# Performance work log

Hardware: AMD Instinct MI355X
Metric: run time of the kernel (lower is better)

The kernel has to match this reference:

```python
import jax, jax.numpy as jnp
import numpy as np

ALPHA = 0.2  # leaky relu slope
NEG_BIG = -9000000000000000.0


def setup_inputs() -> dict:
    key = jax.random.key(0)
    k1, k2, k3, k4 = jax.random.split(key, 4)
    B, N, Fin, Fout = 8, 2048, 256, 256
    h = jax.random.normal(k1, (B, N, Fin), dtype=jnp.float32)
    adj = jax.random.randint(k2, (B, N, N), 0, 2, dtype=jnp.int32)
    # xavier_uniform with gain=1.414
    gain = 1.414
    limW = gain * np.sqrt(6.0 / (Fin + Fout))
    W = jax.random.uniform(k3, (Fin, Fout), dtype=jnp.float32, minval=-limW, maxval=limW)
    lima = gain * np.sqrt(6.0 / (2 * Fout + 1))
    a = jax.random.uniform(k4, (2 * Fout, 1), dtype=jnp.float32, minval=-lima, maxval=lima)
    return {"h": h, "adj": adj, "W": W, "a": a}


def reference(h, adj, W, a):
    # Wh: [B, N, F]
    Wh = jnp.matmul(h, W)
    Fout = W.shape[1]
    a1 = a[:Fout, 0]   # scores for source node i (repeat_interleave side)
    a2 = a[Fout:, 0]   # scores for target node j (repeat side)
    # e[b,i,j] = leakyrelu(Wh[b,i]@a1 + Wh[b,j]@a2)  -- decomposed, no O(N^2 * 2F) tensor
    s1 = jnp.einsum('bnf,f->bn', Wh, a1)  # [B, N]
    s2 = jnp.einsum('bnf,f->bn', Wh, a2)  # [B, N]
    e = jax.nn.leaky_relu(s1[:, :, None] + s2[:, None, :], negative_slope=ALPHA)
    masked = jnp.where(adj > 0, e, jnp.full_like(e, NEG_BIG))
    attention = jax.nn.softmax(masked, axis=2)  # dropout=0 (eval mode)
    h_prime = jnp.matmul(attention, Wh)  # [B, N, F]
    return jax.nn.elu(h_prime)
```

## Files before the change

### kernel.cpp

```cpp
#include <hip/hip_runtime.h>

typedef __attribute__((ext_vector_type(8))) short bhalf8;
typedef __attribute__((ext_vector_type(4))) float floatx4;

#define ALPHA_LR 0.2f

__device__ __forceinline__ unsigned short f2bf(float f) {
  union { float f; unsigned int u; } v; v.f = f;
  unsigned int r = v.u + 0x7fffu + ((v.u >> 16) & 1u);
  return (unsigned short)(r >> 16);
}
__device__ __forceinline__ float bf2f(unsigned short u) {
  union { unsigned int u; float f; } v; v.u = ((unsigned int)u) << 16;
  return v.f;
}
__device__ __forceinline__ void gld16(const void* g, void* l) {
  __builtin_amdgcn_global_load_lds((const __attribute__((address_space(1))) unsigned int*)g,
                                   (__attribute__((address_space(3))) unsigned int*)l,
                                   16, 0, 0);
}

__global__ void k0w_split(const float* __restrict__ W,
                          unsigned short* __restrict__ WThi,
                          unsigned short* __restrict__ WTlo,
                          unsigned int* __restrict__ s2maxEnc) {
  __shared__ float s[16][17];
  const int tx = threadIdx.x, ty = threadIdx.y;
  if (blockIdx.x == 0 && blockIdx.y == 0 && ty == 0 && tx < 8) s2maxEnc[tx] = 0u;
  const int n0 = blockIdx.x * 16, k0 = blockIdx.y * 16;
  s[ty][tx] = W[(k0 + ty) * 256 + n0 + tx];
  __syncthreads();
  float v = s[tx][ty];
  const int k = k0 + tx, n = n0 + ty;
  unsigned short hi = f2bf(v);
  unsigned short lo = f2bf(v - bf2f(hi));
  const int idx = (k >> 5) * 8192 + n * 32 + (k & 31);
  WThi[idx] = hi;
  WTlo[idx] = lo;
}

__global__ __launch_bounds__(256) void k2_pack(const int* __restrict__ adj,
                                               unsigned long long* __restrict__ mask) {
  const int wave = threadIdx.x >> 6, lane = threadIdx.x & 63;
  const long wid = (long)blockIdx.x * 4 + wave;
  const long u0 = wid * 64;
  const int* base = adj + u0 * 64 + lane;
#pragma unroll
  for (int it = 0; it < 64; it += 4) {
    int v0 = base[(it + 0) * 64];
    int v1 = base[(it + 1) * 64];
    int v2 = base[(it + 2) * 64];
    int v3 = base[(it + 3) * 64];
    unsigned long long m0 = __ballot(v0 > 0);
    unsigned long long m1 = __ballot(v1 > 0);
    unsigned long long m2 = __ballot(v2 > 0);
    unsigned long long m3 = __ballot(v3 > 0);
    if (lane == 0) {
      mask[u0 + it + 0] = m0;
      mask[u0 + it + 1] = m1;
      mask[u0 + it + 2] = m2;
      mask[u0 + it + 3] = m3;
    }
  }
}

__global__ __launch_bounds__(512, 2) void k1_mfma(const float* __restrict__ h,
                                                  const unsigned short* __restrict__ Bhi_g,
                                                  const unsigned short* __restrict__ Blo_g,
                                                  const float* __restrict__ a_g,
                                                  unsigned short* __restrict__ WhPack,
                                                  float* __restrict__ s1,
                                                  float* __restrict__ s2,
                                                  unsigned int* __restrict__ s2maxEnc) {
  __shared__ unsigned short Ah[64 * 264], Al[64 * 264];
  __shared__ unsigned short Bh[2][8192], Bl[2][8192];
  __shared__ float s1red[64], s2red[64];
  const int t = threadIdx.x;
  const long r0 = (long)blockIdx.x * 64;
  const int wave = t >> 6, lane = t & 63;

  if (t < 64) { s1red[t] = 0.f; s2red[t] = 0.f; }

#pragma unroll
  for (int rep = 0; rep < 2; rep++) {
    const int off = wave * 1024 + rep * 512;
    gld16(Bhi_g + off + lane * 8, &Bh[0][off]);
    gld16(Blo_g + off + lane * 8, &Bl[0][off]);
  }

#pragma unroll
  for (int q = 0; q < 8; q++) {
    int idx = q * 512 + t;
    int row = idx >> 6, c4 = idx & 63;
    float4 x = *(const float4*)(h + (r0 + row) * 256 + c4 * 4);
    float xs[4] = {x.x, x.y, x.z, x.w};
    unsigned short hs[4], ls[4];
#pragma unroll
    for (int qq = 0; qq < 4; qq++) {
      hs[qq] = f2bf(xs[qq]);
      ls[qq] = f2bf(xs[qq] - bf2f(hs[qq]));
    }
    *(ushort4*)&Ah[row * 264 + c4 * 4] = (ushort4){hs[0], hs[1], hs[2], hs[3]};
    *(ushort4*)&Al[row * 264 + c4 * 4] = (ushort4){ls[0], ls[1], ls[2], ls[3]};
  }
  __syncthreads();

  const int wm = wave >> 2, wn = wave & 3;
  const int lhi = lane >> 4, llo = lane & 15;

  floatx4 acc[2][4];
#pragma unroll
  for (int mt = 0; mt < 2; mt++)
#pragma unroll
    for (int nt = 0; nt < 4; nt++) acc[mt][nt] = (floatx4){0.f, 0.f, 0.f, 0.f};

  for (int ks = 0; ks < 8; ks++) {
    const int cur = ks & 1, nxt = cur ^ 1, ksn = (ks + 1) & 7;
#pragma unroll
    for (int rep = 0; rep < 2; rep++) {
      const int off = wave * 1024 + rep * 512;
      gld16(Bhi_g + ksn * 8192 + off + lane * 8, &Bh[nxt][off]);
      gld16(Blo_g + ksn * 8192 + off + lane * 8, &Bl[nxt][off]);
    }

    const int k0 = ks * 32;
    bhalf8 ah[2], al[2], bh[4], bl[4];
#pragma unroll
    for (int mt = 0; mt < 2; mt++) {
      int ro = (wm * 32 + mt * 16 + llo) * 264 + k0 + lhi * 8;
      ah[mt] = *(const bhalf8*)&Ah[ro];
      al[mt] = *(const bhalf8*)&Al[ro];
    }
#pragma unroll
    for (int nt = 0; nt < 4; nt++) {
      int ro = (wn * 64 + nt * 16 + llo) * 32 + lhi * 8;
      bh[nt] = *(const bhalf8*)&Bh[cur][ro];
      bl[nt] = *(const bhalf8*)&Bl[cur][ro];
    }
#pragma unroll
    for (int mt = 0; mt < 2; mt++)
#pragma unroll
      for (int nt = 0; nt < 4; nt++) {
        acc[mt][nt] = __builtin_amdgcn_mfma_f32_16x16x32_bf16(ah[mt], bh[nt], acc[mt][nt], 0, 0, 0);
        acc[mt][nt] = __builtin_amdgcn_mfma_f32_16x16x32_bf16(ah[mt], bl[nt], acc[mt][nt], 0, 0, 0);
        acc[mt][nt] = __builtin_amdgcn_mfma_f32_16x16x32_bf16(al[mt], bh[nt], acc[mt][nt], 0, 0, 0);
      }
    __syncthreads();
  }

  float a1v[4], a2v[4];
#pragma unroll
  for (int nt = 0; nt < 4; nt++) {
    int f = wn * 64 + nt * 16 + llo;
    a1v[nt] = a_g[f];
    a2v[nt] = a_g[256 + f];
  }

  const int b = (int)(r0 >> 11);
  const int jt_base = (int)((r0 & 2047) >> 5);

#pragma unroll
  for (int mt = 0; mt < 2; mt++) {
    float p1[4], p2[4];
#pragma unroll
    for (int reg = 0; reg < 4; reg++) {
      p1[reg] = acc[mt][0][reg] * a1v[0] + acc[mt][1][reg] * a1v[1] +
                acc[mt][2][reg] * a1v[2] + acc[mt][3][reg] * a1v[3];
      p2[reg] = acc[mt][0][reg] * a2v[0] + acc[mt][1][reg] * a2v[1] +
                acc[mt][2][reg] * a2v[2] + acc[mt][3][reg] * a2v[3];
    }
#pragma unroll
    for (int off = 1; off < 16; off <<= 1) {
#pragma unroll
      for (int reg = 0; reg < 4; reg++) {
        p1[reg] += __shfl_xor(p1[reg], off);
        p2[reg] += __shfl_xor(p2[reg], off);
      }
    }
    if (llo == 0) {
#pragma unroll
      for (int reg = 0; reg < 4; reg++) {
        int il = wm * 32 + mt * 16 + lhi * 4 + reg;
        atomicAdd(&s1red[il], p1[reg]);
        atomicAdd(&s2red[il], p2[reg]);
      }
    }
#pragma unroll
    for (int nt = 0; nt < 4; nt++) {
      int f = wn * 64 + nt * 16 + llo;
      int jt = jt_base + wm;
      ushort4 pk = (ushort4){f2bf(acc[mt][nt][0]), f2bf(acc[mt][nt][1]),
                             f2bf(acc[mt][nt][2]), f2bf(acc[mt][nt][3])};
      *(ushort4*)&WhPack[((long)((b * 64 + jt) * 256 + f)) * 32 + mt * 16 + lhi * 4] = pk;
    }
  }

  __syncthreads();
  if (t < 64) {
    s1[r0 + t] = s1red[t];
    s2[r0 + t] = s2red[t];
    float v = s2red[t];
#pragma unroll
    for (int o = 32; o; o >>= 1) v = fmaxf(v, __shfl_xor(v, o));
    if (t == 0) {
      unsigned int u = __float_as_uint(v);
      unsigned int key = (u & 0x80000000u) ? ~u : (u | 0x80000000u);
      atomicMax(s2maxEnc + b, key);
    }
  }
}

__global__ __launch_bounds__(512, 2) void k3_attn(const unsigned short* __restrict__ WhPack,
                                                  const unsigned int* __restrict__ mask32,
                                                  const float* __restrict__ s1g,
                                                  const float* __restrict__ s2g,
                                                  const unsigned int* __restrict__ s2maxEnc,
                                                  float* __restrict__ out) {
  const int t = threadIdx.x;
  const int lin = blockIdx.x;
  const int b = lin & 7;
  const int ig = lin >> 3;
  const long gr0 = (long)b * 2048 + ig * 64;

  const int wave = t >> 6, lane = t & 63;
  const int rg = wave >> 2, fg = wave & 3;
  const int llo = lane & 15, lhi = lane >> 4;

  __shared__ unsigned short WhL[2][16384];
  __shared__ unsigned short Pl[2][64 * 72];
  __shared__ float s2l[2048];
  __shared__ float lvv[64];

  const int pr = t >> 3;
  const int pq = t & 7;
  const int q2 = pq >> 2;
  const int shq = (pq & 3) * 8;

  const float s1i = s1g[gr0 + pr];
  const unsigned int ek = s2maxEnc[b];
  const float s2max = (ek & 0x80000000u) ? __uint_as_float(ek & 0x7fffffffu)
                                         : __uint_as_float(~ek);
  const float xm = s1i + s2max;
  const float Mi = fmaxf(xm, ALPHA_LR * xm);
  const unsigned int* mrow = mask32 + (gr0 + pr) * 64;

  const int gsrc8 = (((lane & 3) ^ ((lane >> 3) & 3))) * 8;
  const unsigned short* wsrcB =
      WhPack + (long)b * 524288 + wave * 512 + (lane >> 2) * 32 + gsrc8;

  const int boff = fg * 2048 + llo * 32 + (lhi ^ ((llo >> 1) & 3)) * 8;
  const int aoff = (rg * 32 + llo) * 72 + lhi * 8;

  *(float4*)&s2l[t * 4] = *(const float4*)(s2g + (long)b * 2048 + t * 4);
#pragma unroll
  for (int i = 0; i < 4; i++)
    gld16(wsrcB + i * 4096, &WhL[0][i * 4096 + wave * 512]);
  unsigned int m0 = mrow[q2];
  __syncthreads();

  float lsum = 0.f;
  {
    unsigned int mb = m0 >> shq;
    float4 sA = *(const float4*)&s2l[pq * 8];
    float4 sB = *(const float4*)&s2l[pq * 8 + 4];
    float xs[8] = {sA.x, sA.y, sA.z, sA.w, sB.x, sB.y, sB.z, sB.w};
    unsigned int pk[4];
    float e[8];
#pragma unroll
    for (int q = 0; q < 8; q++) {
      float x = s1i + xs[q];
      float lk = fmaxf(x, ALPHA_LR * x);
      float ee = __expf(lk - Mi);
      ee = (mb >> q) & 1u ? ee : 0.f;
      lsum += ee;
      e[q] = ee;
    }
#pragma unroll
    for (int q = 0; q < 4; q++)
      asm("v_cvt_pk_bf16_f32 %0, %1, %2" : "=v"(pk[q]) : "v"(e[2 * q]), "v"(e[2 * q + 1]));
    *(uint4*)&Pl[0][pr * 72 + pq * 8] = (uint4){pk[0], pk[1], pk[2], pk[3]};
  }
  unsigned int mC = mrow[2 + q2];
  __syncthreads();

  floatx4 acc[2][4];
#pragma unroll
  for (int mt = 0; mt < 2; mt++)
#pragma unroll
    for (int nt = 0; nt < 4; nt++) acc[mt][nt] = (floatx4){0.f, 0.f, 0.f, 0.f};

#pragma unroll 2
  for (int step = 0; step < 32; step++) {
    const int cur = step & 1, nxt = cur ^ 1;

    if (step < 31) {
      const long jb = (long)(step + 1) * 16384;
#pragma unroll
      for (int i = 0; i < 4; i++)
        gld16(wsrcB + jb + i * 4096, &WhL[nxt][i * 4096 + wave * 512]);
    }
    unsigned int mN = mrow[(step < 30 ? (step + 2) * 2 : 62) + q2];
    __builtin_amdgcn_sched_barrier(0);

    if (step < 31) {
      unsigned int mb = mC >> shq;
      const int sbase = (step + 1) * 64 + pq * 8;
      float4 sA = *(const float4*)&s2l[sbase];
      float4 sB = *(const float4*)&s2l[sbase + 4];
      float xs[8] = {sA.x, sA.y, sA.z, sA.w, sB.x, sB.y, sB.z, sB.w};
      unsigned int pk[4];
      float e[8];
#pragma unroll
      for (int q = 0; q < 8; q++) {
        float x = s1i + xs[q];
        float lk = fmaxf(x, ALPHA_LR * x);
        float ee = __expf(lk - Mi);
        ee = (mb >> q) & 1u ? ee : 0.f;
        lsum += ee;
        e[q] = ee;
      }
#pragma unroll
      for (int q = 0; q < 4; q++)
        asm("v_cvt_pk_bf16_f32 %0, %1, %2" : "=v"(pk[q]) : "v"(e[2 * q]), "v"(e[2 * q + 1]));
      *(uint4*)&Pl[nxt][pr * 72 + pq * 8] = (uint4){pk[0], pk[1], pk[2], pk[3]};
    }
    mC = mN;

#pragma unroll
    for (int kk = 0; kk < 2; kk++) {
      bhalf8 aF[2], bF[4];
#pragma unroll
      for (int mt = 0; mt < 2; mt++)
        aF[mt] = *(const bhalf8*)&Pl[cur][aoff + mt * 1152 + kk * 32];
#pragma unroll
      for (int nt = 0; nt < 4; nt++)
        bF[nt] = *(const bhalf8*)&WhL[cur][kk * 8192 + nt * 512 + boff];
#pragma unroll
      for (int mt = 0; mt < 2; mt++)
#pragma unroll
        for (int nt = 0; nt < 4; nt++)
          acc[mt][nt] = __builtin_amdgcn_mfma_f32_16x16x32_bf16(aF[mt], bF[nt], acc[mt][nt], 0, 0, 0);
    }

    __syncthreads();
  }

  lsum += __shfl_xor(lsum, 1);
  lsum += __shfl_xor(lsum, 2);
  lsum += __shfl_xor(lsum, 4);
  if ((lane & 7) == 0) lvv[pr] = lsum;
  __syncthreads();

#pragma unroll
  for (int mt = 0; mt < 2; mt++) {
#pragma unroll
    for (int reg = 0; reg < 4; reg++) {
      const int rloc = rg * 32 + mt * 16 + lhi * 4 + reg;
      const float iv = 1.f / fmaxf(lvv[rloc], 1e-35f);
      const long orow = (gr0 + rloc) * 256 + fg * 64 + llo;
#pragma unroll
      for (int nt = 0; nt < 4; nt++) {
        float v = acc[mt][nt][reg] * iv;
        v = v > 0.f ? v : expm1f(v);
        out[orow + nt * 16] = v;
      }
    }
  }
}

extern "C" void kernel_launch(void* const* d_in, const int* in_sizes, int n_in,
                              void* d_out, int out_size, void* d_ws, size_t ws_size,
                              hipStream_t stream) {
  const float* h = (const float*)d_in[0];
  const int* adj = (const int*)d_in[1];
  const float* W = (const float*)d_in[2];
  const float* a = (const float*)d_in[3];
  float* out = (float*)d_out;

  char* ws = (char*)d_ws;
  unsigned short* WhPack = (unsigned short*)ws;
  unsigned short* WThi = (unsigned short*)(ws + 8388608);
  unsigned short* WTlo = (unsigned short*)(ws + 8519680);
  float* s1 = (float*)(ws + 8650752);
  float* s2 = (float*)(ws + 8716288);
  unsigned int* s2maxEnc = (unsigned int*)(ws + 8781824);
  unsigned long long* adjMask = (unsigned long long*)(ws + 8912896);

  hipLaunchKernelGGL(k0w_split, dim3(16, 16), dim3(16, 16), 0, stream, W, WThi, WTlo, s2maxEnc);
  hipLaunchKernelGGL(k1_mfma, dim3(256), dim3(512), 0, stream, h, WThi, WTlo, a,
                     WhPack, s1, s2, s2maxEnc);
  hipLaunchKernelGGL(k2_pack, dim3(2048), dim3(256), 0, stream, adj, adjMask);
  hipLaunchKernelGGL(k3_attn, dim3(256), dim3(512), 0, stream, WhPack,
                     (const unsigned int*)adjMask, s1, s2, s2maxEnc, out);
}
```

Measured before the change: 264.9 us.

## Fuse adjacency mask packing into attention kernel by reading int32 adj directly

Drops the separate kernel that packed the int32 adjacency matrix into bitmasks. The attention kernel now loads the raw int32 adjacency rows with 16-byte vector loads, prefetched two steps ahead, and tests each value directly. This saves one launch plus the write and re-read of the packed mask. In exchange the attention loop now streams 32x more adjacency bytes and holds more live registers for the prefetched int4 values.

```diff
diff --git a/kernel.cpp b/kernel.cpp
--- a/kernel.cpp
+++ b/kernel.cpp
@@ -37,31 +37,6 @@
   const int idx = (k >> 5) * 8192 + n * 32 + (k & 31);
   WThi[idx] = hi;
   WTlo[idx] = lo;
-}
-
-__global__ __launch_bounds__(256) void k2_pack(const int* __restrict__ adj,
-                                               unsigned long long* __restrict__ mask) {
-  const int wave = threadIdx.x >> 6, lane = threadIdx.x & 63;
-  const long wid = (long)blockIdx.x * 4 + wave;
-  const long u0 = wid * 64;
-  const int* base = adj + u0 * 64 + lane;
-#pragma unroll
-  for (int it = 0; it < 64; it += 4) {
-    int v0 = base[(it + 0) * 64];
-    int v1 = base[(it + 1) * 64];
-    int v2 = base[(it + 2) * 64];
-    int v3 = base[(it + 3) * 64];
-    unsigned long long m0 = __ballot(v0 > 0);
-    unsigned long long m1 = __ballot(v1 > 0);
-    unsigned long long m2 = __ballot(v2 > 0);
-    unsigned long long m3 = __ballot(v3 > 0);
-    if (lane == 0) {
-      mask[u0 + it + 0] = m0;
-      mask[u0 + it + 1] = m1;
-      mask[u0 + it + 2] = m2;
-      mask[u0 + it + 3] = m3;
-    }
-  }
 }
 
 __global__ __launch_bounds__(512, 2) void k1_mfma(const float* __restrict__ h,
@@ -211,7 +186,7 @@
 }
 
 __global__ __launch_bounds__(512, 2) void k3_attn(const unsigned short* __restrict__ WhPack,
-                                                  const unsigned int* __restrict__ mask32,
+                                                  const int* __restrict__ adj,
                                                   const float* __restrict__ s1g,
                                                   const float* __restrict__ s2g,
                                                   const unsigned int* __restrict__ s2maxEnc,
@@ -233,8 +208,6 @@
 
   const int pr = t >> 3;
   const int pq = t & 7;
-  const int q2 = pq >> 2;
-  const int shq = (pq & 3) * 8;
 
   const float s1i = s1g[gr0 + pr];
   const unsigned int ek = s2maxEnc[b];
@@ -242,7 +215,7 @@
                                          : __uint_as_float(~ek);
   const float xm = s1i + s2max;
   const float Mi = fmaxf(xm, ALPHA_LR * xm);
-  const unsigned int* mrow = mask32 + (gr0 + pr) * 64;
+  const int* arow = adj + (gr0 + pr) * 2048 + pq * 8;
 
   const int gsrc8 = (((lane & 3) ^ ((lane >> 3) & 3))) * 8;
   const unsigned short* wsrcB =
@@ -255,12 +228,15 @@
 #pragma unroll
   for (int i = 0; i < 4; i++)
     gld16(wsrcB + i * 4096, &WhL[0][i * 4096 + wave * 512]);
-  unsigned int m0 = mrow[q2];
+  int4 a0A = *(const int4*)(arow);
+  int4 a0B = *(const int4*)(arow + 4);
+  int4 ajCA = *(const int4*)(arow + 64);
+  int4 ajCB = *(const int4*)(arow + 68);
   __syncthreads();
 
   float lsum = 0.f;
   {
-    unsigned int mb = m0 >> shq;
+    int am[8] = {a0A.x, a0A.y, a0A.z, a0A.w, a0B.x, a0B.y, a0B.z, a0B.w};
     float4 sA = *(const float4*)&s2l[pq * 8];
     float4 sB = *(const float4*)&s2l[pq * 8 + 4];
     float xs[8] = {sA.x, sA.y, sA.z, sA.w, sB.x, sB.y, sB.z, sB.w};
@@ -271,7 +247,7 @@
       float x = s1i + xs[q];
       float lk = fmaxf(x, ALPHA_LR * x);
       float ee = __expf(lk - Mi);
-      ee = (mb >> q) & 1u ? ee : 0.f;
+      ee = (am[q] > 0) ? ee : 0.f;
       lsum += ee;
       e[q] = ee;
     }
@@ -280,7 +256,6 @@
       asm("v_cvt_pk_bf16_f32 %0, %1, %2" : "=v"(pk[q]) : "v"(e[2 * q]), "v"(e[2 * q + 1]));
     *(uint4*)&Pl[0][pr * 72 + pq * 8] = (uint4){pk[0], pk[1], pk[2], pk[3]};
   }
-  unsigned int mC = mrow[2 + q2];
   __syncthreads();
 
   floatx4 acc[2][4];
@@ -299,11 +274,13 @@
       for (int i = 0; i < 4; i++)
         gld16(wsrcB + jb + i * 4096, &WhL[nxt][i * 4096 + wave * 512]);
     }
-    unsigned int mN = mrow[(step < 30 ? (step + 2) * 2 : 62) + q2];
+    const int tp = (step < 30 ? step + 2 : 31) * 64;
+    int4 ajNA = *(const int4*)(arow + tp);
+    int4 ajNB = *(const int4*)(arow + tp + 4);
     __builtin_amdgcn_sched_barrier(0);
 
     if (step < 31) {
-      unsigned int mb = mC >> shq;
+      int am[8] = {ajCA.x, ajCA.y, ajCA.z, ajCA.w, ajCB.x, ajCB.y, ajCB.z, ajCB.w};
       const int sbase = (step + 1) * 64 + pq * 8;
       float4 sA = *(const float4*)&s2l[sbase];
       float4 sB = *(const float4*)&s2l[sbase + 4];
@@ -315,7 +292,7 @@
         float x = s1i + xs[q];
         float lk = fmaxf(x, ALPHA_LR * x);
         float ee = __expf(lk - Mi);
-        ee = (mb >> q) & 1u ? ee : 0.f;
+        ee = (am[q] > 0) ? ee : 0.f;
         lsum += ee;
         e[q] = ee;
       }
@@ -324,7 +301,7 @@
         asm("v_cvt_pk_bf16_f32 %0, %1, %2" : "=v"(pk[q]) : "v"(e[2 * q]), "v"(e[2 * q + 1]));
       *(uint4*)&Pl[nxt][pr * 72 + pq * 8] = (uint4){pk[0], pk[1], pk[2], pk[3]};
     }
-    mC = mN;
+    ajCA = ajNA; ajCB = ajNB;
 
 #pragma unroll
     for (int kk = 0; kk < 2; kk++) {
@@ -384,12 +361,10 @@
   float* s1 = (float*)(ws + 8650752);
   float* s2 = (float*)(ws + 8716288);
   unsigned int* s2maxEnc = (unsigned int*)(ws + 8781824);
-  unsigned long long* adjMask = (unsigned long long*)(ws + 8912896);
 
   hipLaunchKernelGGL(k0w_split, dim3(16, 16), dim3(16, 16), 0, stream, W, WThi, WTlo, s2maxEnc);
   hipLaunchKernelGGL(k1_mfma, dim3(256), dim3(512), 0, stream, h, WThi, WTlo, a,
                      WhPack, s1, s2, s2maxEnc);
-  hipLaunchKernelGGL(k2_pack, dim3(2048), dim3(256), 0, stream, adj, adjMask);
-  hipLaunchKernelGGL(k3_attn, dim3(256), dim3(512), 0, stream, WhPack,
-                     (const unsigned int*)adjMask, s1, s2, s2maxEnc, out);
-}
+  hipLaunchKernelGGL(k3_attn, dim3(256), dim3(512), 0, stream, WhPack, adj,
+                     s1, s2, s2maxEnc, out);
+}
```

Measured after the change: 243.1 us. 1.09x faster.
